# Optimization experiments

Hardware: AMD Instinct MI355X
Metric: run time of the kernel (lower is better)

Reference implementation:

```python
import jax, jax.numpy as jnp
import numpy as np

V, D, DFF, L, H, N, K, NB, R = 32000, 512, 2048, 4, 8, 64, 8, 32, 64
B, S = 2, 512
DH = D // H


def _layernorm(x, g, b, eps=1e-5):
    m = x.mean(-1, keepdims=True)
    v = ((x - m) ** 2).mean(-1, keepdims=True)
    return (x - m) * jax.lax.rsqrt(v + eps) * g + b


def _forward(input_ids, token_emb, pos_emb, basis_A, basis_emb, recipe,
             Wq, bq, Wk, bk, Wv, bv, Ws, bs, Wup, bup, Wdown, bdown,
             ln1_g, ln1_b, ln2_g, ln2_b, alpha, lnf_g, lnf_b):
    Bc, Sc = input_ids.shape
    x = token_emb[input_ids] + pos_emb[:Sc][None]          # [B,S,D]
    causal = jnp.tril(jnp.ones((Sc, Sc), dtype=bool))
    neg = jnp.asarray(-jnp.inf, x.dtype)
    scale = jnp.asarray(1.0 / np.sqrt(DH), x.dtype)
    for i in range(L):
        rec = recipe[i]                                    # [N,NB]
        neuron_emb = jax.nn.softmax(rec, -1) @ basis_emb   # [N,D] routing embedding
        # ---- SimpleRouter on norm1(x) ----
        n1 = _layernorm(x, ln1_g[i], ln1_b[i])
        q = (n1 @ Wq[i] + bq[i]).reshape(Bc, Sc, H, DH)
        k = (n1 @ Wk[i] + bk[i]).reshape(Bc, Sc, H, DH)
        v = (n1 @ Wv[i] + bv[i]).reshape(Bc, Sc, H, DH)
        attn = jnp.einsum('bqhd,bkhd->bhqk', q, k) * scale
        attn = jnp.where(causal[None, None], attn, neg)
        attn = jax.nn.softmax(attn, -1)
        ctx = jnp.einsum('bhqk,bkhd->bqhd', attn, v).reshape(Bc, Sc, D)
        query = jnp.concatenate([n1, ctx], -1) @ Ws[i] + bs[i]   # [B,S,D]
        scores = query @ neuron_emb.T                            # [B,S,N]
        topk_scores, topk_idx = jax.lax.top_k(scores, K)
        weights = jax.nn.softmax(topk_scores, -1)                # [B,S,K]
        # ---- BasisResidualFFN on norm2(x) ----
        n2 = _layernorm(x, ln2_g[i], ln2_b[i])
        sel = jax.nn.softmax(rec[topk_idx], -1)                  # [B,S,K,NB]
        token_recipe = (sel * weights[..., None]).sum(2)         # [B,S,NB]
        # delta = x @ W_A @ W_A^T with W_A = token_recipe . basis_A, computed
        # WITHOUT materializing [B,S,D,R] (same math, associativity only)
        proj = jnp.einsum('bsd,ndr->bsnr', n2, basis_A)          # [B,S,NB,R]
        h = jnp.einsum('bsn,bsnr->bsr', token_recipe, proj)      # [B,S,R]
        delta = jnp.einsum('bsn,bsr,ndr->bsd', token_recipe, h, basis_A)
        xf = n2 + alpha[i] * delta
        ff = jax.nn.gelu(xf @ Wup[i] + bup[i], approximate=False) @ Wdown[i] + bdown[i]
        x = x + ff                                               # dropout=0 (eval)
    x = _layernorm(x, lnf_g, lnf_b)
    return x @ token_emb.T                                       # tied head


def setup_inputs() -> dict:
    key = jax.random.key(0)
    ks = iter(jax.random.split(key, 40))
    std = 0.02
    nrm = lambda shape, s=std: jax.random.normal(next(ks), shape, jnp.float32) * s
    input_ids = jax.random.randint(next(ks), (B, S), 0, V)
    basis_A = jax.random.normal(next(ks), (NB, D, R), jnp.float32)
    basis_A = basis_A / jnp.linalg.norm(basis_A.reshape(NB, -1), axis=-1)[:, None, None]
    basis_emb = jax.random.normal(next(ks), (NB, D), jnp.float32)
    basis_emb = basis_emb / jnp.linalg.norm(basis_emb, axis=-1, keepdims=True)
    return dict(
        input_ids=input_ids,
        token_emb=nrm((V, D)), pos_emb=nrm((S, D)),
        basis_A=basis_A, basis_emb=basis_emb,
        recipe=jax.random.normal(next(ks), (L, N, NB), jnp.float32) * 0.5,
        Wq=nrm((L, D, D)), bq=jnp.zeros((L, D)),
        Wk=nrm((L, D, D)), bk=jnp.zeros((L, D)),
        Wv=nrm((L, D, D)), bv=jnp.zeros((L, D)),
        Ws=nrm((L, 2 * D, D)), bs=jnp.zeros((L, D)),
        Wup=nrm((L, D, DFF)), bup=jnp.zeros((L, DFF)),
        Wdown=nrm((L, DFF, D)), bdown=jnp.zeros((L, D)),
        ln1_g=jnp.ones((L, D)), ln1_b=jnp.zeros((L, D)),
        ln2_g=jnp.ones((L, D)), ln2_b=jnp.zeros((L, D)),
        alpha=jnp.full((L,), 0.1, jnp.float32),
        lnf_g=jnp.ones((D,)), lnf_b=jnp.zeros((D,)),
    )


def reference(input_ids, token_emb, pos_emb, basis_A, basis_emb, recipe,
              Wq, bq, Wk, bk, Wv, bv, Ws, bs, Wup, bup, Wdown, bdown,
              ln1_g, ln1_b, ln2_g, ln2_b, alpha, lnf_g, lnf_b):
    return _forward(input_ids, token_emb, pos_emb, basis_A, basis_emb, recipe,
                    Wq, bq, Wk, bk, Wv, bv, Ws, bs, Wup, bup, Wdown, bdown,
                    ln1_g, ln1_b, ln2_g, ln2_b, alpha, lnf_g, lnf_b)
```

## Files before the change

kernel.cpp:

```cpp
#include <hip/hip_runtime.h>
#include <hip/hip_bf16.h>
#include <math.h>

#define V_  32000
#define D_  512
#define DFF_ 2048
#define L_  4
#define H_  8
#define N_  64
#define K_  8
#define NB_ 32
#define R_  64
#define B_  2
#define S_  512
#define T_  1024
#define DH_ 64

typedef short bhalf8 __attribute__((ext_vector_type(8)));
typedef float floatx4 __attribute__((ext_vector_type(4)));

#define GLOAD16(gp, lp) __builtin_amdgcn_global_load_lds( \
    (const __attribute__((address_space(1))) void*)(gp), \
    (__attribute__((address_space(3))) void*)(lp), 16, 0, 0)

__device__ __forceinline__ float gelu_f(float v) {
    return 0.5f * v * (1.0f + erff(v * 0.70710678118654752f));
}

__device__ __forceinline__ unsigned pk2(float a, float b) {
    unsigned ua = (unsigned)__bfloat16_as_ushort(__float2bfloat16(a));
    unsigned ub = (unsigned)__bfloat16_as_ushort(__float2bfloat16(b));
    return ua | (ub << 16);
}

template<int BM, int BN, int WR, int WC, int EPI, bool SWAP = false, int SWZ = 0>
__global__ __launch_bounds__(256) void gemm_mfma(
    const __hip_bfloat16* __restrict__ A, int lda, long sA,
    const __hip_bfloat16* __restrict__ Bt, int ldb, long sB,
    const float* __restrict__ bias,
    const float* __restrict__ aux,
    void* __restrict__ Cv, int ldc, long sC,
    int Kdim)
{
    constexpr int FM = BM / WR / 16;
    constexpr int FN = BN / WC / 16;
    constexpr int ACH = BM * 8;
    constexpr int BCH = BN * 8;
    __shared__ __align__(16) short As[2][BM * 64];
    __shared__ __align__(16) short Bs[2][BN * 64];
    const int tid = threadIdx.x;
    const int z = blockIdx.z;
    A  += (long)z * sA;
    Bt += (long)z * sB;
    int bm, bn;
    if constexpr (SWZ == 1) {
        int d = blockIdx.x;
        int xcd = d & 7, k = d >> 3;
        int ty = xcd * 32 + (k >> 3);
        if (ty >= 250) return;
        bm = (k & 7) * BM;
        bn = ty * BN;
    } else {
        bm = (SWAP ? blockIdx.x : blockIdx.y) * BM;
        bn = (SWAP ? blockIdx.y : blockIdx.x) * BN;
    }
    const int w = tid >> 6, lane = tid & 63;
    const int wr = w / WC, wc = w % WC;
    const int moff = wr * (BM / WR), noff = wc * (BN / WC);
    floatx4 acc[FM][FN] = {};

    auto stage = [&](int buf, int k0) {
        #pragma unroll
        for (int i = 0; i < ACH / 256; i++) {
            int c = tid + i * 256;
            int m = c >> 3, u = (c & 7) ^ (m & 7);
            const __hip_bfloat16* src = A + (long)(bm + m) * lda + k0 + u * 8;
            char* dst = (char*)&As[buf][0] + (w * 64 + i * 256) * 16;
            GLOAD16(src, dst);
        }
        #pragma unroll
        for (int i = 0; i < BCH / 256; i++) {
            int c = tid + i * 256;
            int m = c >> 3, u = (c & 7) ^ (m & 7);
            const __hip_bfloat16* src = Bt + (long)(bn + m) * ldb + k0 + u * 8;
            char* dst = (char*)&Bs[buf][0] + (w * 64 + i * 256) * 16;
            GLOAD16(src, dst);
        }
    };

    const int nt = Kdim >> 6;
    stage(0, 0);
    __syncthreads();
    int cur = 0;
    for (int t = 0; t < nt; ++t) {
        if (t + 1 < nt) stage(cur ^ 1, (t + 1) * 64);
        #pragma unroll
        for (int kk = 0; kk < 2; kk++) {
            bhalf8 af[FM], bf[FN];
            #pragma unroll
            for (int fm = 0; fm < FM; fm++) {
                int row = moff + fm * 16 + (lane & 15);
                int u = (kk * 4 + (lane >> 4)) ^ (row & 7);
                af[fm] = *(const bhalf8*)((const char*)&As[cur][0] + row * 128 + u * 16);
            }
            #pragma unroll
            for (int fn = 0; fn < FN; fn++) {
                int row = noff + fn * 16 + (lane & 15);
                int u = (kk * 4 + (lane >> 4)) ^ (row & 7);
                bf[fn] = *(const bhalf8*)((const char*)&Bs[cur][0] + row * 128 + u * 16);
            }
            #pragma unroll
            for (int fm = 0; fm < FM; fm++)
                #pragma unroll
                for (int fn = 0; fn < FN; fn++)
                    acc[fm][fn] = __builtin_amdgcn_mfma_f32_16x16x32_bf16(
                        af[fm], bf[fn], acc[fm][fn], 0, 0, 0);
        }
        __syncthreads();
        cur ^= 1;
    }

    float* Cf = (float*)Cv;
    __hip_bfloat16* Cb = (__hip_bfloat16*)Cv;
    __hip_bfloat16* vtb = (EPI == 5) ? (__hip_bfloat16*)(void*)aux : nullptr;
    const long zoff = (long)z * sC;
    const int lr = lane >> 4, lc = lane & 15;
    float alphaV = (EPI == 3) ? bias[0] : 0.f;
    #pragma unroll
    for (int fm = 0; fm < FM; fm++) {
        #pragma unroll
        for (int fn = 0; fn < FN; fn++) {
            int cN = bn + noff + fn * 16 + lc;
            float bv = (EPI == 3 || !bias) ? 0.f : bias[cN];
            #pragma unroll
            for (int i = 0; i < 4; i++) {
                int rM = bm + moff + fm * 16 + lr * 4 + i;
                long idx = zoff + (long)rM * ldc + cN;
                float v = acc[fm][fn][i] + bv;
                if constexpr (EPI == 0) Cf[idx] = v;
                else if constexpr (EPI == 1) Cb[idx] = __float2bfloat16(v);
                else if constexpr (EPI == 2) Cb[idx] = __float2bfloat16(gelu_f(v));
                else if constexpr (EPI == 3)
                    Cb[idx] = __float2bfloat16(aux[idx] + alphaV * acc[fm][fn][i]);
                else if constexpr (EPI == 4) Cf[idx] += v;
                else if constexpr (EPI == 5) {
                    __hip_bfloat16 bvv = __float2bfloat16(v);
                    Cb[idx] = bvv;
                    if (cN >= 1024) {
                        int hh = (cN - 1024) >> 6, dh = (cN - 1024) & 63;
                        int bb = rM >> 9, ss = rM & 511;
                        vtb[(((long)bb * 8 + hh) * 64 + dh) * 512 + ss] = bvv;
                    }
                }
            }
        }
    }
}

__global__ __launch_bounds__(256) void attn_mfma(
    const __hip_bfloat16* __restrict__ qkv,
    const __hip_bfloat16* __restrict__ vt,
    __hip_bfloat16* __restrict__ catB)
{
    __shared__ short pbuf[4][16][72];
    const int tid = threadIdx.x;
    const int w = tid >> 6, lane = tid & 63;
    const int g = lane >> 4, ql = lane & 15;
    const int h = blockIdx.y, b = blockIdx.z;
    const int qbase = blockIdx.x * 64 + w * 16;

    const long qrow = ((long)(b * S_ + qbase + ql)) * 1536 + h * DH_;
    bhalf8 qa0 = *(const bhalf8*)(qkv + qrow + g * 8);
    bhalf8 qa1 = *(const bhalf8*)(qkv + qrow + 32 + g * 8);
    const __hip_bfloat16* kB = qkv + 512;
    const __hip_bfloat16* vbase = vt + ((long)(b * H_ + h)) * DH_ * S_;

    floatx4 o[4] = {};
    float m = -INFINITY, ls = 0.f;
    const float SC = 0.125f * 1.44269504088896f;
    const int nblk = blockIdx.x + 1;

    for (int kvb = 0; kvb < nblk; kvb++) {
        const int kb0 = kvb * 64;
        floatx4 st[4];
        #pragma unroll
        for (int t = 0; t < 4; t++) {
            long krow = ((long)(b * S_ + kb0 + t * 16 + ql)) * 1536 + h * DH_;
            bhalf8 ka0 = *(const bhalf8*)(kB + krow + g * 8);
            bhalf8 ka1 = *(const bhalf8*)(kB + krow + 32 + g * 8);
            floatx4 z = {};
            z = __builtin_amdgcn_mfma_f32_16x16x32_bf16(ka0, qa0, z, 0, 0, 0);
            z = __builtin_amdgcn_mfma_f32_16x16x32_bf16(ka1, qa1, z, 0, 0, 0);
            st[t] = z;
        }
        const int q = qbase + ql;
        float p[4][4];
        float m4 = -INFINITY;
        #pragma unroll
        for (int t = 0; t < 4; t++)
            #pragma unroll
            for (int i = 0; i < 4; i++) {
                int kv = kb0 + t * 16 + g * 4 + i;
                float v = (kv <= q) ? st[t][i] * SC : -INFINITY;
                p[t][i] = v; m4 = fmaxf(m4, v);
            }
        m4 = fmaxf(m4, __shfl_xor(m4, 16));
        m4 = fmaxf(m4, __shfl_xor(m4, 32));
        float mnew = fmaxf(m, m4);
        float corr = exp2f(m - mnew);
        m = mnew;
        float lsum = 0.f;
        #pragma unroll
        for (int t = 0; t < 4; t++)
            #pragma unroll
            for (int i = 0; i < 4; i++) {
                float e = exp2f(p[t][i] - mnew);
                p[t][i] = e; lsum += e;
            }
        lsum += __shfl_xor(lsum, 16);
        lsum += __shfl_xor(lsum, 32);
        ls = ls * corr + lsum;
        unsigned* prow = (unsigned*)&pbuf[w][ql][0];
        #pragma unroll
        for (int t = 0; t < 4; t++) {
            prow[t * 8 + g * 2]     = pk2(p[t][0], p[t][1]);
            prow[t * 8 + g * 2 + 1] = pk2(p[t][2], p[t][3]);
        }
        #pragma unroll
        for (int i = 0; i < 4; i++) {
            float c = __shfl(corr, g * 4 + i);
            #pragma unroll
            for (int dt = 0; dt < 4; dt++) o[dt][i] *= c;
        }
        __syncthreads();
        #pragma unroll
        for (int ks = 0; ks < 2; ks++) {
            bhalf8 pa = *(const bhalf8*)&pbuf[w][ql][ks * 32 + g * 8];
            #pragma unroll
            for (int dt = 0; dt < 4; dt++) {
                bhalf8 vb = *(const bhalf8*)(vbase + (long)(dt * 16 + ql) * S_ + kb0 + ks * 32 + g * 8);
                o[dt] = __builtin_amdgcn_mfma_f32_16x16x32_bf16(pa, vb, o[dt], 0, 0, 0);
            }
        }
        __syncthreads();
    }
    const float inv = 1.f / ls;
    #pragma unroll
    for (int i = 0; i < 4; i++) {
        float iv = __shfl(inv, g * 4 + i);
        int trow = b * S_ + qbase + g * 4 + i;
        #pragma unroll
        for (int dt = 0; dt < 4; dt++)
            catB[(long)trow * 1024 + 512 + h * DH_ + dt * 16 + ql] =
                __float2bfloat16(o[dt][i] * iv);
    }
}

__device__ __forceinline__ void tcvt_dev(const float* in, int ldn, long sIn,
                                         __hip_bfloat16* out, int ldk, long sOut,
                                         int bx, int by, int bz, float (*tsh)[33]) {
    in  += (long)bz * sIn;
    out += (long)bz * sOut;
    int k0 = by * 32, n0 = bx * 32;
    int tx = threadIdx.x & 31, ty = threadIdx.x >> 5;
    #pragma unroll
    for (int r = 0; r < 4; r++) tsh[ty * 4 + r][tx] = in[(long)(k0 + ty * 4 + r) * ldn + n0 + tx];
    __syncthreads();
    #pragma unroll
    for (int r = 0; r < 4; r++)
        out[(long)(n0 + ty * 4 + r) * ldk + k0 + tx] = __float2bfloat16(tsh[tx][ty * 4 + r]);
}

__global__ __launch_bounds__(256) void prologue_kernel(
    const float* __restrict__ temb, __hip_bfloat16* __restrict__ tembB,
    const float* __restrict__ basisA, __hip_bfloat16* __restrict__ projT,
    __hip_bfloat16* __restrict__ deltaT,
    const float* __restrict__ bq, const float* __restrict__ bk,
    const float* __restrict__ bv, float* __restrict__ bqkv,
    const float* __restrict__ Wq, const float* __restrict__ Wk,
    const float* __restrict__ Wv, __hip_bfloat16* __restrict__ qkvT,
    const float* __restrict__ Ws, __hip_bfloat16* __restrict__ WsT,
    const float* __restrict__ Wup, __hip_bfloat16* __restrict__ WupT,
    const float* __restrict__ Wdn, __hip_bfloat16* __restrict__ WdnT,
    const int* __restrict__ ids, const float* __restrict__ pemb,
    float* __restrict__ x)
{
    __shared__ float tsh[32][33];
    const int blk = blockIdx.x, tid = threadIdx.x;
    if (blk < 16000) {
        long i = ((long)blk * 256 + tid) * 4;
        float4 v = *(const float4*)(temb + i);
        tembB[i]     = __float2bfloat16(v.x);
        tembB[i + 1] = __float2bfloat16(v.y);
        tembB[i + 2] = __float2bfloat16(v.z);
        tembB[i + 3] = __float2bfloat16(v.w);
    } else if (blk < 20096) {
        long i = (long)(blk - 16000) * 256 + tid;
        int r = i & 63; int d = (i >> 6) & 511; int n = i >> 15;
        __hip_bfloat16 v = __float2bfloat16(basisA[i]);
        projT[((long)n * R_ + r) * D_ + d] = v;
        deltaT[(long)d * (NB_ * R_) + n * R_ + r] = v;
    } else if (blk < 20120) {
        int i = (blk - 20096) * 256 + tid;
        int l = i / 1536, j = i % 1536;
        float v = (j < 512) ? bq[l * 512 + j] : (j < 1024) ? bk[l * 512 + j - 512]
                                                           : bv[l * 512 + j - 1024];
        bqkv[i] = v;
    } else if (blk < 21144) {
        int lin = blk - 20120;
        tcvt_dev(Wq, D_, (long)D_ * D_, qkvT, D_, (long)1536 * D_,
                 lin & 15, (lin >> 4) & 15, lin >> 8, tsh);
    } else if (blk < 22168) {
        int lin = blk - 21144;
        tcvt_dev(Wk, D_, (long)D_ * D_, qkvT + 512 * 512, D_, (long)1536 * D_,
                 lin & 15, (lin >> 4) & 15, lin >> 8, tsh);
    } else if (blk < 23192) {
        int lin = blk - 22168;
        tcvt_dev(Wv, D_, (long)D_ * D_, qkvT + 1024 * 512, D_, (long)1536 * D_,
                 lin & 15, (lin >> 4) & 15, lin >> 8, tsh);
    } else if (blk < 25240) {
        int lin = blk - 23192;
        tcvt_dev(Ws, D_, (long)2 * D_ * D_, WsT, 2 * D_, (long)2 * D_ * D_,
                 lin & 15, (lin >> 4) & 31, lin >> 9, tsh);
    } else if (blk < 29336) {
        int lin = blk - 25240;
        tcvt_dev(Wup, DFF_, (long)D_ * DFF_, WupT, D_, (long)D_ * DFF_,
                 lin & 63, (lin >> 6) & 15, lin >> 10, tsh);
    } else if (blk < 33432) {
        int lin = blk - 29336;
        tcvt_dev(Wdn, D_, (long)DFF_ * D_, WdnT, DFF_, (long)DFF_ * D_,
                 lin & 15, (lin >> 4) & 63, lin >> 10, tsh);
    } else {
        int t = blk - 33432;
        int s = t % S_;
        int id = ids[t];
        for (int d = tid; d < D_; d += 256)
            x[(long)t * D_ + d] = temb[(long)id * D_ + d] + pemb[(long)s * D_ + d];
    }
}

__device__ __forceinline__ void ln_dev(const float* row, const float* g, const float* b,
                                       float* outf, __hip_bfloat16* outb, int ldo,
                                       long t, float* red) {
    int tid = threadIdx.x;
    float v0 = row[tid], v1 = row[tid + 256];
    red[tid] = v0 + v1; __syncthreads();
    for (int off = 128; off; off >>= 1) { if (tid < off) red[tid] += red[tid + off]; __syncthreads(); }
    float mean = red[0] * (1.0f / D_); __syncthreads();
    float d0 = v0 - mean, d1 = v1 - mean;
    red[tid] = d0 * d0 + d1 * d1; __syncthreads();
    for (int off = 128; off; off >>= 1) { if (tid < off) red[tid] += red[tid + off]; __syncthreads(); }
    float rstd = rsqrtf(red[0] * (1.0f / D_) + 1e-5f);
    float o0 = d0 * rstd * g[tid]       + b[tid];
    float o1 = d1 * rstd * g[tid + 256] + b[tid + 256];
    if (outf) {
        outf[t * D_ + tid]       = o0;
        outf[t * D_ + tid + 256] = o1;
    }
    outb[t * ldo + tid]       = __float2bfloat16(o0);
    outb[t * ldo + tid + 256] = __float2bfloat16(o1);
}

__global__ __launch_bounds__(256) void prep_kernel(
    const float* __restrict__ x,
    const float* __restrict__ ln1g, const float* __restrict__ ln1b,
    const float* __restrict__ ln2g, const float* __restrict__ ln2b,
    const float* __restrict__ rec, const float* __restrict__ bemb,
    __hip_bfloat16* __restrict__ catB, float* __restrict__ buf1,
    __hip_bfloat16* __restrict__ n2B,
    __hip_bfloat16* __restrict__ neb, float* __restrict__ sel)
{
    __shared__ float red[256];
    int blk = blockIdx.x;
    if (blk < 1024) {
        ln_dev(x + (long)blk * D_, ln1g, ln1b, nullptr, catB, 1024, blk, red);
    } else if (blk < 2048) {
        long t = blk - 1024;
        ln_dev(x + t * D_, ln2g, ln2b, buf1, n2B, 512, t, red);
    } else {
        int n = blk - 2048;
        __shared__ float wsm[NB_];
        if (threadIdx.x == 0) {
            float mx = -1e30f;
            for (int i = 0; i < NB_; i++) mx = fmaxf(mx, rec[n * NB_ + i]);
            float sm = 0.f;
            for (int i = 0; i < NB_; i++) { float e = expf(rec[n * NB_ + i] - mx); wsm[i] = e; sm += e; }
            float inv = 1.f / sm;
            for (int i = 0; i < NB_; i++) wsm[i] *= inv;
        }
        __syncthreads();
        if (threadIdx.x < NB_) sel[n * NB_ + threadIdx.x] = wsm[threadIdx.x];
        for (int d = threadIdx.x; d < D_; d += 256) {
            float acc = 0.f;
            #pragma unroll
            for (int nb = 0; nb < NB_; nb++) acc += wsm[nb] * bemb[nb * D_ + d];
            neb[(long)n * D_ + d] = __float2bfloat16(acc);
        }
    }
}

__global__ __launch_bounds__(256) void ln_kernel(const float* __restrict__ in,
                                                 const float* __restrict__ g,
                                                 const float* __restrict__ b,
                                                 __hip_bfloat16* __restrict__ outb) {
    __shared__ float red[256];
    long t = blockIdx.x;
    ln_dev(in + t * D_, g, b, nullptr, outb, 512, t, red);
}

__global__ __launch_bounds__(64) void route_kernel(const float* __restrict__ scores,
                                                   const float* __restrict__ sel,
                                                   float* __restrict__ tr) {
    int t = blockIdx.x, lane = threadIdx.x;
    float myval = scores[(long)t * N_ + lane];
    float topv[K_]; int topi[K_];
    #pragma unroll
    for (int kk = 0; kk < K_; kk++) {
        float v = myval; int idx = lane;
        #pragma unroll
        for (int off = 32; off; off >>= 1) {
            float ov = __shfl_down(v, off);
            int oi = __shfl_down(idx, off);
            if (ov > v || (ov == v && oi < idx)) { v = ov; idx = oi; }
        }
        v = __shfl(v, 0); idx = __shfl(idx, 0);
        topv[kk] = v; topi[kk] = idx;
        if (lane == idx) myval = -INFINITY;
    }
    float mx = topv[0];
    float w[K_], sum = 0.f;
    #pragma unroll
    for (int kk = 0; kk < K_; kk++) { w[kk] = expf(topv[kk] - mx); sum += w[kk]; }
    float inv = 1.f / sum;
    if (lane < NB_) {
        float acc = 0.f;
        #pragma unroll
        for (int kk = 0; kk < K_; kk++) acc += w[kk] * inv * sel[topi[kk] * NB_ + lane];
        tr[(long)t * NB_ + lane] = acc;
    }
}

__global__ __launch_bounds__(256) void hg_kernel(const float* __restrict__ tr,
                                                 const float* __restrict__ P,
                                                 __hip_bfloat16* __restrict__ g) {
    int t = blockIdx.x, tid = threadIdx.x;
    __shared__ float hl[64];
    __shared__ float trl[32];
    if (tid < 32) trl[tid] = tr[(long)t * 32 + tid];
    __syncthreads();
    if (tid < 64) {
        float acc = 0.f;
        const float* p = P + (long)t * 2048 + tid;
        #pragma unroll
        for (int n = 0; n < 32; n++) acc += trl[n] * p[n * 64];
        hl[tid] = acc;
    }
    __syncthreads();
    #pragma unroll
    for (int j = 0; j < 8; j++) {
        int idx = tid * 8 + j;
        int n = idx >> 6, r = idx & 63;
        g[(long)t * 2048 + idx] = __float2bfloat16(trl[n] * hl[r]);
    }
}

extern "C" void kernel_launch(void* const* d_in, const int* in_sizes, int n_in,
                              void* d_out, int out_size, void* d_ws, size_t ws_size,
                              hipStream_t stream) {
    const int*   ids    = (const int*)d_in[0];
    const float* temb   = (const float*)d_in[1];
    const float* pemb   = (const float*)d_in[2];
    const float* basisA = (const float*)d_in[3];
    const float* bemb   = (const float*)d_in[4];
    const float* recipe = (const float*)d_in[5];
    const float* Wq = (const float*)d_in[6],  *bq = (const float*)d_in[7];
    const float* Wk = (const float*)d_in[8],  *bk = (const float*)d_in[9];
    const float* Wv = (const float*)d_in[10], *bv = (const float*)d_in[11];
    const float* Ws = (const float*)d_in[12], *bs = (const float*)d_in[13];
    const float* Wup = (const float*)d_in[14], *bup = (const float*)d_in[15];
    const float* Wdn = (const float*)d_in[16], *bdn = (const float*)d_in[17];
    const float* ln1g = (const float*)d_in[18], *ln1b = (const float*)d_in[19];
    const float* ln2g = (const float*)d_in[20], *ln2b = (const float*)d_in[21];
    const float* alpha = (const float*)d_in[22];
    const float* lnfg = (const float*)d_in[23], *lnfb = (const float*)d_in[24];
    float* out = (float*)d_out;
    float* W = (float*)d_ws;

    float* x    = W + 0;
    float* buf1 = W + 524288;
    float* scb  = W + 1048576;
    float* trb  = W + 1114112;
    float* sel  = W + 1212416;
    float* P    = W + 1214464;
    float* bqkv = W + 3835904;
    __hip_bfloat16* SB = (__hip_bfloat16*)(W + 3844096);
    __hip_bfloat16* tembB  = SB + 0;
    __hip_bfloat16* qkvT   = SB + 16384000;
    __hip_bfloat16* WsT    = SB + 19529728;
    __hip_bfloat16* WupT   = SB + 21626880;
    __hip_bfloat16* WdnT   = SB + 25821184;
    __hip_bfloat16* projT  = SB + 30015488;
    __hip_bfloat16* deltaT = SB + 31064064;
    __hip_bfloat16* neB    = SB + 32112640;
    __hip_bfloat16* catB   = SB + 32145408;
    __hip_bfloat16* qryB   = SB + 33193984;
    __hip_bfloat16* n2B    = SB + 33718272;
    __hip_bfloat16* xfB    = SB + 34242560;
    __hip_bfloat16* gB     = SB + 34766848;
    __hip_bfloat16* ffhB   = SB + 36864000;
    __hip_bfloat16* qkvB   = SB + 38961152;
    __hip_bfloat16* VtB    = SB + 40534016;

    dim3 blk(256);
    prologue_kernel<<<34456, blk, 0, stream>>>(
        temb, tembB, basisA, projT, deltaT, bq, bk, bv, bqkv,
        Wq, Wk, Wv, qkvT, Ws, WsT, Wup, WupT, Wdn, WdnT, ids, pemb, x);

    for (int l = 0; l < L_; l++) {
        prep_kernel<<<2112, blk, 0, stream>>>(
            x, ln1g + l * D_, ln1b + l * D_, ln2g + l * D_, ln2b + l * D_,
            recipe + (long)l * N_ * NB_, bemb, catB, buf1, n2B, neB, sel);
        gemm_mfma<64, 64, 2, 2, 5><<<dim3(24, 16), blk, 0, stream>>>(
            catB, 1024, 0, qkvT + (long)l * 1536 * 512, D_, 0, bqkv + l * 1536,
            (const float*)VtB, qkvB, 1536, 0, D_);
        attn_mfma<<<dim3(8, H_, B_), blk, 0, stream>>>(qkvB, VtB, catB);
        gemm_mfma<64, 64, 2, 2, 1><<<dim3(8, 16), blk, 0, stream>>>(
            catB, 2 * D_, 0, WsT + (long)l * 2 * D_ * D_, 2 * D_, 0, bs + l * D_, nullptr,
            qryB, D_, 0, 2 * D_);
        gemm_mfma<128, 64, 2, 2, 0><<<dim3(1, 8), blk, 0, stream>>>(
            qryB, D_, 0, neB, D_, 0, nullptr, nullptr, scb, N_, 0, D_);
        route_kernel<<<T_, dim3(64), 0, stream>>>(scb, sel, trb);
        gemm_mfma<128, 64, 2, 2, 0><<<dim3(1, 8, NB_), blk, 0, stream>>>(
            n2B, D_, 0, projT, D_, (long)R_ * D_, nullptr, nullptr, P, NB_ * R_, R_, D_);
        hg_kernel<<<T_, blk, 0, stream>>>(trb, P, gB);
        gemm_mfma<64, 64, 2, 2, 3><<<dim3(8, 16), blk, 0, stream>>>(
            gB, NB_ * R_, 0, deltaT, NB_ * R_, 0, alpha + l, buf1,
            xfB, D_, 0, NB_ * R_);
        gemm_mfma<64, 64, 2, 2, 2><<<dim3(32, 16), blk, 0, stream>>>(
            xfB, D_, 0, WupT + (long)l * D_ * DFF_, D_, 0, bup + l * DFF_, nullptr,
            ffhB, DFF_, 0, D_);
        gemm_mfma<64, 64, 2, 2, 4><<<dim3(8, 16), blk, 0, stream>>>(
            ffhB, DFF_, 0, WdnT + (long)l * DFF_ * D_, DFF_, 0, bdn + l * D_, nullptr,
            x, D_, 0, DFF_);
    }
    ln_kernel<<<T_, blk, 0, stream>>>(x, lnfg, lnfb, n2B);
    gemm_mfma<128, 128, 2, 2, 0, false, 1><<<dim3(2048), blk, 0, stream>>>(
        n2B, D_, 0, tembB, D_, 0, nullptr, nullptr, out, V_, 0, D_);
}
```

Measured before the change: 623.4 us.

## Fold router projection into Ws·neuron_emb, split-K atomic GEMMs, retile LM head

Precomputes Ws·neuron_embᵀ and bs·neuron_embᵀ per layer in the prep kernel, so the query GEMM plus score GEMM become one split-K GEMM over the concatenated input that atomically accumulates directly into the router scores. The route and hg kernels are merged, and the Wdown GEMM uses a 2-way split-K with atomicAdd into x. The final vocab projection switches from 128x128 to 128x64 tiles with a generalized XCD swizzle. This removes a full D-wide intermediate and two launches, at the cost of per-layer weight folding work inside prep, atomic contention and nondeterministic float summation order.

```diff
diff --git a/kernel.cpp b/kernel.cpp
--- a/kernel.cpp
+++ b/kernel.cpp
@@ -54,11 +54,14 @@
     Bt += (long)z * sB;
     int bm, bn;
     if constexpr (SWZ == 1) {
+        constexpr int MT = T_ / BM;
+        constexpr int NP = V_ / BN;
+        constexpr int PPX = (NP + 7) / 8;
         int d = blockIdx.x;
         int xcd = d & 7, k = d >> 3;
-        int ty = xcd * 32 + (k >> 3);
-        if (ty >= 250) return;
-        bm = (k & 7) * BM;
+        int ty = xcd * PPX + (k >> 3);
+        if (ty >= NP) return;
+        bm = (k & (MT - 1)) * BM;
         bn = ty * BN;
     } else {
         bm = (SWAP ? blockIdx.x : blockIdx.y) * BM;
@@ -131,7 +134,7 @@
         #pragma unroll
         for (int fn = 0; fn < FN; fn++) {
             int cN = bn + noff + fn * 16 + lc;
-            float bv = (EPI == 3 || !bias) ? 0.f : bias[cN];
+            float bv = (EPI == 3 || !bias || (EPI == 6 && z != 0)) ? 0.f : bias[cN];
             #pragma unroll
             for (int i = 0; i < 4; i++) {
                 int rM = bm + moff + fm * 16 + lr * 4 + i;
@@ -152,6 +155,7 @@
                         vtb[(((long)bb * 8 + hh) * 64 + dh) * 512 + ss] = bvv;
                     }
                 }
+                else if constexpr (EPI == 6) atomicAdd(&Cf[idx], v);
             }
         }
     }
@@ -279,7 +283,6 @@
     const float* __restrict__ bv, float* __restrict__ bqkv,
     const float* __restrict__ Wq, const float* __restrict__ Wk,
     const float* __restrict__ Wv, __hip_bfloat16* __restrict__ qkvT,
-    const float* __restrict__ Ws, __hip_bfloat16* __restrict__ WsT,
     const float* __restrict__ Wup, __hip_bfloat16* __restrict__ WupT,
     const float* __restrict__ Wdn, __hip_bfloat16* __restrict__ WdnT,
     const int* __restrict__ ids, const float* __restrict__ pemb,
@@ -318,20 +321,16 @@
         int lin = blk - 22168;
         tcvt_dev(Wv, D_, (long)D_ * D_, qkvT + 1024 * 512, D_, (long)1536 * D_,
                  lin & 15, (lin >> 4) & 15, lin >> 8, tsh);
-    } else if (blk < 25240) {
+    } else if (blk < 27288) {
         int lin = blk - 23192;
-        tcvt_dev(Ws, D_, (long)2 * D_ * D_, WsT, 2 * D_, (long)2 * D_ * D_,
-                 lin & 15, (lin >> 4) & 31, lin >> 9, tsh);
-    } else if (blk < 29336) {
-        int lin = blk - 25240;
         tcvt_dev(Wup, DFF_, (long)D_ * DFF_, WupT, D_, (long)D_ * DFF_,
                  lin & 63, (lin >> 6) & 15, lin >> 10, tsh);
-    } else if (blk < 33432) {
-        int lin = blk - 29336;
+    } else if (blk < 31384) {
+        int lin = blk - 27288;
         tcvt_dev(Wdn, D_, (long)DFF_ * D_, WdnT, DFF_, (long)DFF_ * D_,
                  lin & 15, (lin >> 4) & 63, lin >> 10, tsh);
     } else {
-        int t = blk - 33432;
+        int t = blk - 31384;
         int s = t % S_;
         int id = ids[t];
         for (int d = tid; d < D_; d += 256)
@@ -366,36 +365,65 @@
     const float* __restrict__ ln1g, const float* __restrict__ ln1b,
     const float* __restrict__ ln2g, const float* __restrict__ ln2b,
     const float* __restrict__ rec, const float* __restrict__ bemb,
+    const float* __restrict__ Ws, const float* __restrict__ bs,
     __hip_bfloat16* __restrict__ catB, float* __restrict__ buf1,
     __hip_bfloat16* __restrict__ n2B,
-    __hip_bfloat16* __restrict__ neb, float* __restrict__ sel)
+    __hip_bfloat16* __restrict__ WsneT, float* __restrict__ bsne,
+    float* __restrict__ sel, float* __restrict__ scb)
 {
     __shared__ float red[256];
-    int blk = blockIdx.x;
+    int blk = blockIdx.x, tid = threadIdx.x;
     if (blk < 1024) {
         ln_dev(x + (long)blk * D_, ln1g, ln1b, nullptr, catB, 1024, blk, red);
     } else if (blk < 2048) {
         long t = blk - 1024;
         ln_dev(x + t * D_, ln2g, ln2b, buf1, n2B, 512, t, red);
+    } else if (blk < 2304) {
+        int local = blk - 2048;
+        int rg = local >> 2, ng = local & 3;
+        __shared__ float wsm2[16][32];
+        __shared__ float nesh[16][512];
+        if (tid < 16) {
+            int n = ng * 16 + tid;
+            float mx = -1e30f;
+            for (int i = 0; i < 32; i++) mx = fmaxf(mx, rec[n * 32 + i]);
+            float sm = 0.f;
+            for (int i = 0; i < 32; i++) { float e = expf(rec[n * 32 + i] - mx); wsm2[tid][i] = e; sm += e; }
+            float inv = 1.f / sm;
+            for (int i = 0; i < 32; i++) wsm2[tid][i] *= inv;
+        }
+        __syncthreads();
+        if (rg == 0 && tid < 16 * 32)
+            sel[(ng * 16 + (tid >> 5)) * 32 + (tid & 31)] = wsm2[tid >> 5][tid & 31];
+        #pragma unroll
+        for (int j = 0; j < 32; j++) {
+            int idx = tid + j * 256;
+            int nl = idx >> 9, d = idx & 511;
+            float a = 0.f;
+            #pragma unroll
+            for (int nb = 0; nb < 32; nb++) a += wsm2[nl][nb] * bemb[nb * 512 + d];
+            nesh[nl][d] = a;
+        }
+        __syncthreads();
+        if (rg == 0 && tid < 16) {
+            float a = 0.f;
+            const float* ne = nesh[tid];
+            for (int d = 0; d < 512; d++) a += bs[d] * ne[d];
+            bsne[ng * 16 + tid] = a;
+        }
+        {
+            int r = rg * 16 + (tid >> 4), nl = tid & 15;
+            const float* wrow = Ws + (long)r * 512;
+            const float* ne = nesh[nl];
+            float a = 0.f;
+            for (int d = 0; d < 512; d++) a += wrow[d] * ne[d];
+            WsneT[(ng * 16 + nl) * 1024 + r] = __float2bfloat16(a);
+        }
     } else {
-        int n = blk - 2048;
-        __shared__ float wsm[NB_];
-        if (threadIdx.x == 0) {
-            float mx = -1e30f;
-            for (int i = 0; i < NB_; i++) mx = fmaxf(mx, rec[n * NB_ + i]);
-            float sm = 0.f;
-            for (int i = 0; i < NB_; i++) { float e = expf(rec[n * NB_ + i] - mx); wsm[i] = e; sm += e; }
-            float inv = 1.f / sm;
-            for (int i = 0; i < NB_; i++) wsm[i] *= inv;
-        }
-        __syncthreads();
-        if (threadIdx.x < NB_) sel[n * NB_ + threadIdx.x] = wsm[threadIdx.x];
-        for (int d = threadIdx.x; d < D_; d += 256) {
-            float acc = 0.f;
-            #pragma unroll
-            for (int nb = 0; nb < NB_; nb++) acc += wsm[nb] * bemb[nb * D_ + d];
-            neb[(long)n * D_ + d] = __float2bfloat16(acc);
-        }
+        int local = blk - 2304;
+        float4* p = (float4*)(scb + (long)local * 1024);
+        float4 zz = {0.f, 0.f, 0.f, 0.f};
+        p[tid] = zz;
     }
 }
 
@@ -408,45 +436,42 @@
     ln_dev(in + t * D_, g, b, nullptr, outb, 512, t, red);
 }
 
-__global__ __launch_bounds__(64) void route_kernel(const float* __restrict__ scores,
-                                                   const float* __restrict__ sel,
-                                                   float* __restrict__ tr) {
-    int t = blockIdx.x, lane = threadIdx.x;
-    float myval = scores[(long)t * N_ + lane];
-    float topv[K_]; int topi[K_];
-    #pragma unroll
-    for (int kk = 0; kk < K_; kk++) {
-        float v = myval; int idx = lane;
-        #pragma unroll
-        for (int off = 32; off; off >>= 1) {
-            float ov = __shfl_down(v, off);
-            int oi = __shfl_down(idx, off);
-            if (ov > v || (ov == v && oi < idx)) { v = ov; idx = oi; }
-        }
-        v = __shfl(v, 0); idx = __shfl(idx, 0);
-        topv[kk] = v; topi[kk] = idx;
-        if (lane == idx) myval = -INFINITY;
-    }
-    float mx = topv[0];
-    float w[K_], sum = 0.f;
-    #pragma unroll
-    for (int kk = 0; kk < K_; kk++) { w[kk] = expf(topv[kk] - mx); sum += w[kk]; }
-    float inv = 1.f / sum;
-    if (lane < NB_) {
-        float acc = 0.f;
-        #pragma unroll
-        for (int kk = 0; kk < K_; kk++) acc += w[kk] * inv * sel[topi[kk] * NB_ + lane];
-        tr[(long)t * NB_ + lane] = acc;
-    }
-}
-
-__global__ __launch_bounds__(256) void hg_kernel(const float* __restrict__ tr,
-                                                 const float* __restrict__ P,
-                                                 __hip_bfloat16* __restrict__ g) {
+__global__ __launch_bounds__(256) void route_hg(
+    const float* __restrict__ scb, const float* __restrict__ sel,
+    const float* __restrict__ P, __hip_bfloat16* __restrict__ g)
+{
     int t = blockIdx.x, tid = threadIdx.x;
+    __shared__ float trl[32];
     __shared__ float hl[64];
-    __shared__ float trl[32];
-    if (tid < 32) trl[tid] = tr[(long)t * 32 + tid];
+    if (tid < 64) {
+        int lane = tid;
+        float myval = scb[(long)t * N_ + lane];
+        float topv[K_]; int topi[K_];
+        #pragma unroll
+        for (int kk = 0; kk < K_; kk++) {
+            float v = myval; int idx = lane;
+            #pragma unroll
+            for (int off = 32; off; off >>= 1) {
+                float ov = __shfl_down(v, off);
+                int oi = __shfl_down(idx, off);
+                if (ov > v || (ov == v && oi < idx)) { v = ov; idx = oi; }
+            }
+            v = __shfl(v, 0); idx = __shfl(idx, 0);
+            topv[kk] = v; topi[kk] = idx;
+            if (lane == idx) myval = -INFINITY;
+        }
+        float mx = topv[0];
+        float w[K_], sum = 0.f;
+        #pragma unroll
+        for (int kk = 0; kk < K_; kk++) { w[kk] = expf(topv[kk] - mx); sum += w[kk]; }
+        float inv = 1.f / sum;
+        if (lane < NB_) {
+            float a = 0.f;
+            #pragma unroll
+            for (int kk = 0; kk < K_; kk++) a += w[kk] * inv * sel[topi[kk] * NB_ + lane];
+            trl[lane] = a;
+        }
+    }
     __syncthreads();
     if (tid < 64) {
         float acc = 0.f;
@@ -489,21 +514,19 @@
     float* x    = W + 0;
     float* buf1 = W + 524288;
     float* scb  = W + 1048576;
-    float* trb  = W + 1114112;
+    float* bsne = W + 1114112;
     float* sel  = W + 1212416;
     float* P    = W + 1214464;
     float* bqkv = W + 3835904;
     __hip_bfloat16* SB = (__hip_bfloat16*)(W + 3844096);
     __hip_bfloat16* tembB  = SB + 0;
     __hip_bfloat16* qkvT   = SB + 16384000;
-    __hip_bfloat16* WsT    = SB + 19529728;
+    __hip_bfloat16* WsneT  = SB + 19529728;
     __hip_bfloat16* WupT   = SB + 21626880;
     __hip_bfloat16* WdnT   = SB + 25821184;
     __hip_bfloat16* projT  = SB + 30015488;
     __hip_bfloat16* deltaT = SB + 31064064;
-    __hip_bfloat16* neB    = SB + 32112640;
     __hip_bfloat16* catB   = SB + 32145408;
-    __hip_bfloat16* qryB   = SB + 33193984;
     __hip_bfloat16* n2B    = SB + 33718272;
     __hip_bfloat16* xfB    = SB + 34242560;
     __hip_bfloat16* gB     = SB + 34766848;
@@ -512,38 +535,36 @@
     __hip_bfloat16* VtB    = SB + 40534016;
 
     dim3 blk(256);
-    prologue_kernel<<<34456, blk, 0, stream>>>(
+    prologue_kernel<<<32408, blk, 0, stream>>>(
         temb, tembB, basisA, projT, deltaT, bq, bk, bv, bqkv,
-        Wq, Wk, Wv, qkvT, Ws, WsT, Wup, WupT, Wdn, WdnT, ids, pemb, x);
+        Wq, Wk, Wv, qkvT, Wup, WupT, Wdn, WdnT, ids, pemb, x);
 
     for (int l = 0; l < L_; l++) {
-        prep_kernel<<<2112, blk, 0, stream>>>(
+        prep_kernel<<<2368, blk, 0, stream>>>(
             x, ln1g + l * D_, ln1b + l * D_, ln2g + l * D_, ln2b + l * D_,
-            recipe + (long)l * N_ * NB_, bemb, catB, buf1, n2B, neB, sel);
+            recipe + (long)l * N_ * NB_, bemb,
+            Ws + (long)l * 2 * D_ * D_, bs + l * D_,
+            catB, buf1, n2B, WsneT, bsne, sel, scb);
         gemm_mfma<64, 64, 2, 2, 5><<<dim3(24, 16), blk, 0, stream>>>(
             catB, 1024, 0, qkvT + (long)l * 1536 * 512, D_, 0, bqkv + l * 1536,
             (const float*)VtB, qkvB, 1536, 0, D_);
         attn_mfma<<<dim3(8, H_, B_), blk, 0, stream>>>(qkvB, VtB, catB);
-        gemm_mfma<64, 64, 2, 2, 1><<<dim3(8, 16), blk, 0, stream>>>(
-            catB, 2 * D_, 0, WsT + (long)l * 2 * D_ * D_, 2 * D_, 0, bs + l * D_, nullptr,
-            qryB, D_, 0, 2 * D_);
-        gemm_mfma<128, 64, 2, 2, 0><<<dim3(1, 8), blk, 0, stream>>>(
-            qryB, D_, 0, neB, D_, 0, nullptr, nullptr, scb, N_, 0, D_);
-        route_kernel<<<T_, dim3(64), 0, stream>>>(scb, sel, trb);
+        gemm_mfma<128, 64, 2, 2, 6><<<dim3(1, 8, 4), blk, 0, stream>>>(
+            catB, 1024, 256, WsneT, 1024, 256, bsne, nullptr, scb, N_, 0, 256);
         gemm_mfma<128, 64, 2, 2, 0><<<dim3(1, 8, NB_), blk, 0, stream>>>(
             n2B, D_, 0, projT, D_, (long)R_ * D_, nullptr, nullptr, P, NB_ * R_, R_, D_);
-        hg_kernel<<<T_, blk, 0, stream>>>(trb, P, gB);
+        route_hg<<<T_, blk, 0, stream>>>(scb, sel, P, gB);
         gemm_mfma<64, 64, 2, 2, 3><<<dim3(8, 16), blk, 0, stream>>>(
             gB, NB_ * R_, 0, deltaT, NB_ * R_, 0, alpha + l, buf1,
             xfB, D_, 0, NB_ * R_);
         gemm_mfma<64, 64, 2, 2, 2><<<dim3(32, 16), blk, 0, stream>>>(
             xfB, D_, 0, WupT + (long)l * D_ * DFF_, D_, 0, bup + l * DFF_, nullptr,
             ffhB, DFF_, 0, D_);
-        gemm_mfma<64, 64, 2, 2, 4><<<dim3(8, 16), blk, 0, stream>>>(
-            ffhB, DFF_, 0, WdnT + (long)l * DFF_ * D_, DFF_, 0, bdn + l * D_, nullptr,
-            x, D_, 0, DFF_);
+        gemm_mfma<64, 64, 2, 2, 6><<<dim3(8, 16, 2), blk, 0, stream>>>(
+            ffhB, DFF_, 1024, WdnT + (long)l * DFF_ * D_, DFF_, 1024, bdn + l * D_, nullptr,
+            x, D_, 0, 1024);
     }
     ln_kernel<<<T_, blk, 0, stream>>>(x, lnfg, lnfb, n2B);
-    gemm_mfma<128, 128, 2, 2, 0, false, 1><<<dim3(2048), blk, 0, stream>>>(
+    gemm_mfma<128, 64, 2, 2, 0, false, 1><<<dim3(4032), blk, 0, stream>>>(
         n2B, D_, 0, tembB, D_, 0, nullptr, nullptr, out, V_, 0, D_);
 }
```

Result: slower. 1.072 ms (+71.9%).
